# Optimization experiments

Measured on AMD Instinct MI355X. Metric: run time of the kernel, lower is better.

## Reference

```python
import jax, jax.numpy as jnp
import numpy as np

N = 100000          # number of nodes (queries == sources here)
DEG = 32            # uniform neighbor count
E = N * DEG         # total edges
C_IN = 8
HID = 32
C_OUT = 32


def setup_inputs() -> dict:
    key = jax.random.key(0)
    k1, k2, k3, k4, k5 = jax.random.split(key, 5)
    in_features = jax.random.normal(k1, (N, C_IN), dtype=jnp.float32)
    in_weights = jax.random.uniform(k2, (N,), dtype=jnp.float32)
    # MLP: Linear(2*C_IN -> HID), GELU, Linear(HID -> C_OUT)
    W1 = jax.random.normal(k3, (2 * C_IN, HID), dtype=jnp.float32) / np.sqrt(2 * C_IN)
    b1 = jnp.zeros((HID,), dtype=jnp.float32)
    W2 = jax.random.normal(k4, (HID, C_OUT), dtype=jnp.float32) / np.sqrt(HID)
    b2 = jnp.zeros((C_OUT,), dtype=jnp.float32)
    neighbor_index = jax.random.randint(k5, (E,), 0, N, dtype=jnp.int64)
    row_splits = (jnp.arange(N + 1, dtype=jnp.int64) * DEG)  # uniform CSR splits
    return {"in_features": in_features, "in_weights": in_weights,
            "W1": W1, "b1": b1, "W2": W2, "b2": b2,
            "neighbor_index": neighbor_index, "row_splits": row_splits}


def reference(in_features, in_weights, W1, b1, W2, b2, neighbor_index, row_splits):
    num_edges = neighbor_index.shape[0]
    num_out = row_splits.shape[0] - 1  # M output nodes
    # segment id of each edge (== repeat_interleave of node ids by row counts)
    seg = jnp.searchsorted(row_splits, jnp.arange(num_edges), side="right") - 1
    gathered = in_features[neighbor_index]          # [E, C_in] neighbor gather
    self_feats = in_features[seg]                   # [E, C_in] repeated self features
    agg = jnp.concatenate([gathered, self_feats], axis=1)  # [E, 2*C_in]
    h = jax.nn.gelu(agg @ W1 + b1)                  # [E, HID]
    h = h @ W2 + b2                                 # [E, C_out]
    h = in_weights[neighbor_index][:, None] * h     # quadrature weighting
    sums = jax.ops.segment_sum(h, seg, num_segments=num_out)  # segment_csr sum
    counts = (row_splits[1:] - row_splits[:-1]).astype(h.dtype)
    out = sums / jnp.maximum(counts, 1)[:, None]    # reduce='mean'
    return out
```

## Files before the change

kernel.cpp:

```cpp
#include <hip/hip_runtime.h>

#define DEG 32
#define HID 32
#define CIN 8

typedef float v2f __attribute__((ext_vector_type(2)));
typedef short bf16x8 __attribute__((ext_vector_type(8)));
typedef float f32x16 __attribute__((ext_vector_type(16)));

#define GELU_A ((float)(2.0 * 1.4426950408889634 * 0.7978845608028654))
#define GELU_B ((float)(2.0 * 1.4426950408889634 * 0.7978845608028654 * 0.044715))

__device__ __forceinline__ unsigned f2bf(float f) {
    unsigned b = __float_as_uint(f);
    return (b + 0x7fffu + ((b >> 16) & 1u)) >> 16;
}
__device__ __forceinline__ unsigned pack2(float lo, float hi) {
    return f2bf(lo) | (f2bf(hi) << 16);
}

__global__ __launch_bounds__(256) void precompute_xw(
    const float* __restrict__ x, const float* __restrict__ W1,
    const float* __restrict__ W2, unsigned* __restrict__ x16,
    unsigned* __restrict__ w1f, unsigned* __restrict__ w2f, int N) {
    int tid = blockIdx.x * 256 + threadIdx.x;
    if (blockIdx.x == 0) {
        int t = threadIdx.x;
        if (t < 64) {
            int kb = (t >> 5) * 8, col = t & 31;
            uint4 o;
            o.x = pack2(W1[(kb + 0) * HID + col], W1[(kb + 1) * HID + col]);
            o.y = pack2(W1[(kb + 2) * HID + col], W1[(kb + 3) * HID + col]);
            o.z = pack2(W1[(kb + 4) * HID + col], W1[(kb + 5) * HID + col]);
            o.w = pack2(W1[(kb + 6) * HID + col], W1[(kb + 7) * HID + col]);
            *(uint4*)(w1f + t * 4) = o;
        } else if (t < 192) {
            int u = t - 64;
            int f = u >> 6, l = u & 63;
            int kb = f * 16 + ((l >> 5) * 8), col = l & 31;
            uint4 o;
            o.x = pack2(W2[(kb + 0) * HID + col], W2[(kb + 1) * HID + col]);
            o.y = pack2(W2[(kb + 2) * HID + col], W2[(kb + 3) * HID + col]);
            o.z = pack2(W2[(kb + 4) * HID + col], W2[(kb + 5) * HID + col]);
            o.w = pack2(W2[(kb + 6) * HID + col], W2[(kb + 7) * HID + col]);
            *(uint4*)(w2f + (f * 64 + l) * 4) = o;
        }
    }
    if (tid < N) {
        const float4* xp = (const float4*)(x + (size_t)tid * CIN);
        float4 a = xp[0], b = xp[1];
        uint4 o;
        o.x = pack2(a.x, a.y);  o.y = pack2(a.z, a.w);
        o.z = pack2(b.x, b.y);  o.w = pack2(b.z, b.w);
        *(uint4*)(x16 + (size_t)tid * 4) = o;
    }
}

__device__ __forceinline__ float gelu_reduce(const f32x16& acc, const float* swp,
                                             float b1v) {
    v2f gacc = {0.f, 0.f};
#pragma unroll
    for (int q = 0; q < 4; ++q) {
        float4 wq = *(const float4*)(swp + 8 * q);
#pragma unroll
        for (int h = 0; h < 2; ++h) {
            int i = q * 4 + h * 2;
            v2f tt = {acc[i] + b1v, acc[i + 1] + b1v};
            v2f x2 = tt * tt;
            v2f zz = tt * (x2 * (-GELU_B) + (-GELU_A));
            v2f ee;
            ee.x = __builtin_amdgcn_exp2f(zz.x);  ee.y = __builtin_amdgcn_exp2f(zz.y);
            v2f dd = ee + 1.0f;
            v2f rr;
            rr.x = __builtin_amdgcn_rcpf(dd.x);   rr.y = __builtin_amdgcn_rcpf(dd.y);
            v2f wp = h ? (v2f){wq.z, wq.w} : (v2f){wq.x, wq.y};
            gacc += wp * (tt * rr);
        }
    }
    float g = gacc.x + gacc.y;
    g += __shfl_xor(g, 32);
    return g;
}

__global__ __launch_bounds__(512, 4) void git_fused(
    const unsigned* __restrict__ x16, const unsigned* __restrict__ w1f,
    const unsigned* __restrict__ w2f, const float* __restrict__ wgt,
    const float* __restrict__ b1, const float* __restrict__ b2,
    const int* __restrict__ nbr, float* __restrict__ out, int N) {
    __shared__ float sw[8 * 64];
    __shared__ __align__(16) unsigned short sg[2432];

    int t = threadIdx.x;
    int wv = t >> 6;
    int l  = t & 63;
    int l5 = l & 31;
    int hi = l >> 5;
    int nb = blockIdx.x * 16 + wv * 2;

    int n0 = min(nb + 0, N - 1), n1 = min(nb + 1, N - 1);

    int   J = nbr[(hi ? n1 : n0) * DEG + l5];
    float W = wgt[J];
    int jsw = __shfl_xor(J, 32);

    const bf16x8* x16v = (const bf16x8*)x16;
    bf16x8 A0 = x16v[hi ? n0 : J];
    bf16x8 A1 = x16v[hi ? n1 : jsw];
    bf16x8 bfrag = *((const bf16x8*)w1f + l);
    float myb1 = b1[l5];

    float* swv = &sw[wv * 64];
    swv[hi * 32 + l5] = W;

    float ws = W;
    ws += __shfl_xor(ws, 1);  ws += __shfl_xor(ws, 2);
    ws += __shfl_xor(ws, 4);  ws += __shfl_xor(ws, 8);
    ws += __shfl_xor(ws, 16);

    f32x16 z0 = {}, z1 = {};
    f32x16 a0 = __builtin_amdgcn_mfma_f32_32x32x16_bf16(A0, bfrag, z0, 0, 0, 0);
    f32x16 a1 = __builtin_amdgcn_mfma_f32_32x32x16_bf16(A1, bfrag, z1, 0, 0, 0);

    float g0 = gelu_reduce(a0, swv + hi * 4,      myb1);
    float g1 = gelu_reduce(a1, swv + 32 + hi * 4, myb1);

    unsigned short* sgw = &sg[wv * 160];
    float ga = hi ? g1 : g0;
    sgw[hi * 40 + l5] = (unsigned short)f2bf(ga);

    bf16x8 eb1 = *((const bf16x8*)w2f + l);
    bf16x8 eb2 = *((const bf16x8*)w2f + 64 + l);
    float myb2 = b2[l5];
    const char* sgb = (const char*)sgw;
    bf16x8 ea1 = *(const bf16x8*)(sgb + l5 * 80 + hi * 16);
    bf16x8 ea2 = *(const bf16x8*)(sgb + l5 * 80 + 32 + hi * 16);
    f32x16 zz = {};
    f32x16 acc = __builtin_amdgcn_mfma_f32_32x32x16_bf16(ea1, eb1, zz, 0, 0, 0);
    acc = __builtin_amdgcn_mfma_f32_32x32x16_bf16(ea2, eb2, acc, 0, 0, 0);

    float wsx = __shfl_xor(ws, 32);
    if (hi == 0) {
        if (nb < N)
            out[(size_t)n0 * HID + l5] = fmaf(ws,  myb2, acc[0]) * (1.0f / DEG);
        if (nb + 1 < N)
            out[(size_t)n1 * HID + l5] = fmaf(wsx, myb2, acc[1]) * (1.0f / DEG);
    }
}

__global__ __launch_bounds__(256) void fused_fallback(
    const float* __restrict__ x, const float* __restrict__ wgt,
    const float* __restrict__ W1, const float* __restrict__ b1,
    const float* __restrict__ W2, const float* __restrict__ b2,
    const int* __restrict__ nbr, float* __restrict__ out, int N) {
    __shared__ float sW2[HID * HID];
    __shared__ float sb2[HID];
    __shared__ int2  sp[8 * DEG];
    int t = threadIdx.x;
#pragma unroll
    for (int i = 0; i < 4; ++i) sW2[t + i * 256] = W2[t + i * 256];
    if (t < HID) sb2[t] = b2[t];
    int slot = t >> 5, hid = t & 31;
    int node = blockIdx.x * 8 + slot;
    bool valid = node < N;
    int nc = valid ? node : (N - 1);
    int   j_own = nbr[nc * DEG + hid];
    float w_own = wgt[j_own];
    sp[slot * DEG + hid] = make_int2(j_own * (CIN * 4), __float_as_int(w_own));
    const float4* xip = (const float4*)(x + (size_t)nc * CIN);
    float4 xa = xip[0], xb = xip[1];
    float w1t[8];
#pragma unroll
    for (int k = 0; k < 8; ++k) w1t[k] = W1[k * HID + hid];
    float vb = b1[hid];
    vb = fmaf(xa.x, W1[ 8 * HID + hid], vb);
    vb = fmaf(xa.y, W1[ 9 * HID + hid], vb);
    vb = fmaf(xa.z, W1[10 * HID + hid], vb);
    vb = fmaf(xa.w, W1[11 * HID + hid], vb);
    vb = fmaf(xb.x, W1[12 * HID + hid], vb);
    vb = fmaf(xb.y, W1[13 * HID + hid], vb);
    vb = fmaf(xb.z, W1[14 * HID + hid], vb);
    vb = fmaf(xb.w, W1[15 * HID + hid], vb);
    float ws = w_own;
    ws += __shfl_xor(ws, 1);  ws += __shfl_xor(ws, 2);
    ws += __shfl_xor(ws, 4);  ws += __shfl_xor(ws, 8);
    ws += __shfl_xor(ws, 16);
    __syncthreads();
    const char* xbytes = (const char*)x;
    const int2* myp = &sp[slot * DEG];
    float g = 0.f;
#pragma unroll 8
    for (int e = 0; e < DEG; ++e) {
        int2  p  = myp[e];
        float wjv = __int_as_float(p.y);
        const float4* xjp = (const float4*)(xbytes + (unsigned)p.x);
        float4 a = xjp[0], b = xjp[1];
        float tin = vb;
        tin = fmaf(a.x, w1t[0], tin); tin = fmaf(a.y, w1t[1], tin);
        tin = fmaf(a.z, w1t[2], tin); tin = fmaf(a.w, w1t[3], tin);
        tin = fmaf(b.x, w1t[4], tin); tin = fmaf(b.y, w1t[5], tin);
        tin = fmaf(b.z, w1t[6], tin); tin = fmaf(b.w, w1t[7], tin);
        float x2 = tin * tin;
        float z  = tin * fmaf(GELU_B, x2, GELU_A);
        float e2 = __builtin_amdgcn_exp2f(z);
        float r  = __builtin_amdgcn_rcpf(1.0f + e2);
        g = fmaf(wjv, fmaf(-tin, r, tin), g);
    }
    float acc = 0.f;
#pragma unroll
    for (int h = 0; h < HID; ++h) {
        float gh = __shfl(g, h, 32);
        acc = fmaf(gh, sW2[h * HID + hid], acc);
    }
    if (valid) out[(size_t)node * HID + hid] = fmaf(ws, sb2[hid], acc) * (1.0f / DEG);
}

extern "C" void kernel_launch(void* const* d_in, const int* in_sizes, int n_in,
                              void* d_out, int out_size, void* d_ws, size_t ws_size,
                              hipStream_t stream) {
    const float* x   = (const float*)d_in[0];
    const float* wq  = (const float*)d_in[1];
    const float* W1  = (const float*)d_in[2];
    const float* b1  = (const float*)d_in[3];
    const float* W2  = (const float*)d_in[4];
    const float* b2  = (const float*)d_in[5];
    const int*   nbr = (const int*)d_in[6];
    float* out = (float*)d_out;

    int N = in_sizes[1];

    size_t off_x16 = 0;
    size_t off_w1  = (off_x16 + (size_t)N * 16 + 255) & ~(size_t)255;
    size_t off_w2  = off_w1 + 1024;
    size_t need    = off_w2 + 2048;

    if (ws_size >= need) {
        unsigned* x16 = (unsigned*)((char*)d_ws + off_x16);
        unsigned* w1f = (unsigned*)((char*)d_ws + off_w1);
        unsigned* w2f = (unsigned*)((char*)d_ws + off_w2);

        int blocks_pre = (N + 255) / 256;
        precompute_xw<<<blocks_pre, 256, 0, stream>>>(x, W1, W2, x16, w1f, w2f, N);

        int blocks_main = (N + 15) / 16;
        git_fused<<<blocks_main, 512, 0, stream>>>(x16, w1f, w2f, wq, b1, b2,
                                                   nbr, out, N);
    } else {
        int blocks = (N + 7) / 8;
        fused_fallback<<<blocks, 256, 0, stream>>>(x, wq, W1, b1, W2, b2, nbr, out, N);
    }
}
```

Baseline: 114.9 us.

## Process four node pairs per wave with software-prefetched gathers

Each wave now handles eight nodes in four iterations instead of two nodes. The neighbor-index loads for all iterations are issued up front, and the next pair's weight and feature gathers are prefetched while the current pair's MFMA and GELU run. Blocks shrink to 256 threads covering 32 nodes, and the weight fragments and biases are loaded once per wave. The aim is to hide gather latency and amortize setup, at the cost of more registers and fewer waves in flight. The per-wave shared-memory scratch for the second GEMM input is reused across iterations without an explicit barrier.

```diff
diff --git a/kernel.cpp b/kernel.cpp
--- a/kernel.cpp
+++ b/kernel.cpp
@@ -82,12 +82,12 @@
     return g;
 }
 
-__global__ __launch_bounds__(512, 4) void git_fused(
+__global__ __launch_bounds__(256) void git_fused(
     const unsigned* __restrict__ x16, const unsigned* __restrict__ w1f,
     const unsigned* __restrict__ w2f, const float* __restrict__ wgt,
     const float* __restrict__ b1, const float* __restrict__ b2,
     const int* __restrict__ nbr, float* __restrict__ out, int N) {
-    __shared__ float sw[8 * 64];
+    __shared__ float sw[4 * 2 * 64];
     __shared__ __align__(16) unsigned short sg[2432];
 
     int t = threadIdx.x;
@@ -95,55 +95,76 @@
     int l  = t & 63;
     int l5 = l & 31;
     int hi = l >> 5;
-    int nb = blockIdx.x * 16 + wv * 2;
-
-    int n0 = min(nb + 0, N - 1), n1 = min(nb + 1, N - 1);
-
-    int   J = nbr[(hi ? n1 : n0) * DEG + l5];
-    float W = wgt[J];
-    int jsw = __shfl_xor(J, 32);
+    int nb = blockIdx.x * 32 + wv * 8;
 
     const bf16x8* x16v = (const bf16x8*)x16;
-    bf16x8 A0 = x16v[hi ? n0 : J];
-    bf16x8 A1 = x16v[hi ? n1 : jsw];
     bf16x8 bfrag = *((const bf16x8*)w1f + l);
+    bf16x8 eb1   = *((const bf16x8*)w2f + l);
+    bf16x8 eb2   = *((const bf16x8*)w2f + 64 + l);
     float myb1 = b1[l5];
-
-    float* swv = &sw[wv * 64];
-    swv[hi * 32 + l5] = W;
-
-    float ws = W;
-    ws += __shfl_xor(ws, 1);  ws += __shfl_xor(ws, 2);
-    ws += __shfl_xor(ws, 4);  ws += __shfl_xor(ws, 8);
-    ws += __shfl_xor(ws, 16);
-
-    f32x16 z0 = {}, z1 = {};
-    f32x16 a0 = __builtin_amdgcn_mfma_f32_32x32x16_bf16(A0, bfrag, z0, 0, 0, 0);
-    f32x16 a1 = __builtin_amdgcn_mfma_f32_32x32x16_bf16(A1, bfrag, z1, 0, 0, 0);
-
-    float g0 = gelu_reduce(a0, swv + hi * 4,      myb1);
-    float g1 = gelu_reduce(a1, swv + 32 + hi * 4, myb1);
+    float myb2 = b2[l5];
+
+    int J[4];
+#pragma unroll
+    for (int k = 0; k < 4; ++k) {
+        int n0 = min(nb + 2 * k,     N - 1);
+        int n1 = min(nb + 2 * k + 1, N - 1);
+        J[k] = nbr[(hi ? n1 : n0) * DEG + l5];
+    }
+
+    float W = wgt[J[0]];
+    int jsw0 = __shfl_xor(J[0], 32);
+    bf16x8 A0 = x16v[hi ? min(nb,     N - 1) : J[0]];
+    bf16x8 A1 = x16v[hi ? min(nb + 1, N - 1) : jsw0];
 
     unsigned short* sgw = &sg[wv * 160];
-    float ga = hi ? g1 : g0;
-    sgw[hi * 40 + l5] = (unsigned short)f2bf(ga);
-
-    bf16x8 eb1 = *((const bf16x8*)w2f + l);
-    bf16x8 eb2 = *((const bf16x8*)w2f + 64 + l);
-    float myb2 = b2[l5];
     const char* sgb = (const char*)sgw;
-    bf16x8 ea1 = *(const bf16x8*)(sgb + l5 * 80 + hi * 16);
-    bf16x8 ea2 = *(const bf16x8*)(sgb + l5 * 80 + 32 + hi * 16);
-    f32x16 zz = {};
-    f32x16 acc = __builtin_amdgcn_mfma_f32_32x32x16_bf16(ea1, eb1, zz, 0, 0, 0);
-    acc = __builtin_amdgcn_mfma_f32_32x32x16_bf16(ea2, eb2, acc, 0, 0, 0);
-
-    float wsx = __shfl_xor(ws, 32);
-    if (hi == 0) {
-        if (nb < N)
-            out[(size_t)n0 * HID + l5] = fmaf(ws,  myb2, acc[0]) * (1.0f / DEG);
-        if (nb + 1 < N)
-            out[(size_t)n1 * HID + l5] = fmaf(wsx, myb2, acc[1]) * (1.0f / DEG);
+
+#pragma unroll
+    for (int k = 0; k < 4; ++k) {
+        float  Wn = 0.f;
+        bf16x8 A0n = {}, A1n = {};
+        if (k < 3) {
+            Wn = wgt[J[k + 1]];
+            int jswn = __shfl_xor(J[k + 1], 32);
+            A0n = x16v[hi ? min(nb + 2 * k + 2, N - 1) : J[k + 1]];
+            A1n = x16v[hi ? min(nb + 2 * k + 3, N - 1) : jswn];
+        }
+
+        float* swv = &sw[wv * 128 + (k & 1) * 64];
+        swv[hi * 32 + l5] = W;
+
+        float ws = W;
+        ws += __shfl_xor(ws, 1);  ws += __shfl_xor(ws, 2);
+        ws += __shfl_xor(ws, 4);  ws += __shfl_xor(ws, 8);
+        ws += __shfl_xor(ws, 16);
+
+        f32x16 z0 = {}, z1 = {};
+        f32x16 a0 = __builtin_amdgcn_mfma_f32_32x32x16_bf16(A0, bfrag, z0, 0, 0, 0);
+        f32x16 a1 = __builtin_amdgcn_mfma_f32_32x32x16_bf16(A1, bfrag, z1, 0, 0, 0);
+
+        float g0 = gelu_reduce(a0, swv + hi * 4,      myb1);
+        float g1 = gelu_reduce(a1, swv + 32 + hi * 4, myb1);
+
+        float ga = hi ? g1 : g0;
+        sgw[hi * 40 + l5] = (unsigned short)f2bf(ga);
+
+        bf16x8 ea1 = *(const bf16x8*)(sgb + l5 * 80 + hi * 16);
+        bf16x8 ea2 = *(const bf16x8*)(sgb + l5 * 80 + 32 + hi * 16);
+        f32x16 zz = {};
+        f32x16 acc = __builtin_amdgcn_mfma_f32_32x32x16_bf16(ea1, eb1, zz, 0, 0, 0);
+        acc = __builtin_amdgcn_mfma_f32_32x32x16_bf16(ea2, eb2, acc, 0, 0, 0);
+
+        float wsx = __shfl_xor(ws, 32);
+        if (hi == 0) {
+            int n0 = nb + 2 * k, n1 = nb + 2 * k + 1;
+            if (n0 < N)
+                out[(size_t)n0 * HID + l5] = fmaf(ws,  myb2, acc[0]) * (1.0f / DEG);
+            if (n1 < N)
+                out[(size_t)n1 * HID + l5] = fmaf(wsx, myb2, acc[1]) * (1.0f / DEG);
+        }
+
+        W = Wn;  A0 = A0n;  A1 = A1n;
     }
 }
 
@@ -241,8 +262,8 @@
         int blocks_pre = (N + 255) / 256;
         precompute_xw<<<blocks_pre, 256, 0, stream>>>(x, W1, W2, x16, w1f, w2f, N);
 
-        int blocks_main = (N + 15) / 16;
-        git_fused<<<blocks_main, 512, 0, stream>>>(x16, w1f, w2f, wq, b1, b2,
+        int blocks_main = (N + 31) / 32;
+        git_fused<<<blocks_main, 256, 0, stream>>>(x16, w1f, w2f, wq, b1, b2,
                                                    nbr, out, N);
     } else {
         int blocks = (N + 7) / 8;
```

New measurement: 116.2 us. About the same (+1.1%).
